# Optimization experiments

Hardware: AMD Instinct MI355X
Metric: run time of the kernel (lower is better)

Reference implementation:

```python
import jax, jax.numpy as jnp
import numpy as np

B, T, C, H = 2, 2048, 2048, 16
HD = C // H  # head dim = 128
ROPE_BASE = 10000.0


def apply_rope(x):
    # x: [B, T, H, HD]; interleaved-pair rotation as in torchtune RoPE
    t = x.shape[1]
    half = x.shape[-1] // 2
    theta = 1.0 / (ROPE_BASE ** (jnp.arange(0, HD, 2, dtype=jnp.float32) / HD))  # [HD/2]
    ang = jnp.arange(t, dtype=jnp.float32)[:, None] * theta[None, :]  # [T, HD/2]
    cos = jnp.cos(ang)[None, :, None, :]  # [1, T, 1, HD/2]
    sin = jnp.sin(ang)[None, :, None, :]
    xs = x.reshape(*x.shape[:-1], half, 2)  # [B,T,H,HD/2,2]
    x0, x1 = xs[..., 0], xs[..., 1]
    out = jnp.stack([x0 * cos - x1 * sin, x1 * cos + x0 * sin], axis=-1)
    return out.reshape(x.shape)


def setup_inputs() -> dict:
    key = jax.random.key(0)
    k1, k2, k3 = jax.random.split(key, 3)
    x = jax.random.normal(k1, (B, T, C), dtype=jnp.float32)
    attn_mask = jnp.tril(jnp.ones((T, T), dtype=bool))[None, None]  # causal [1,1,T,T]
    W_attn = jax.random.normal(k2, (3 * C, C), dtype=jnp.float32) * (C ** -0.5)
    W_proj = jax.random.normal(k3, (C, C), dtype=jnp.float32) * (C ** -0.5)
    return {"x": x, "attn_mask": attn_mask, "W_attn": W_attn, "W_proj": W_proj}


def reference(x, attn_mask, W_attn, W_proj):
    b, t, c = x.shape
    qkv = x @ W_attn.T  # [B,T,3C]
    q, k, v = jnp.split(qkv, 3, axis=-1)
    q = apply_rope(q.reshape(b, t, H, HD)).transpose(0, 2, 1, 3)  # [B,H,T,HD]
    k = apply_rope(k.reshape(b, t, H, HD)).transpose(0, 2, 1, 3)
    v = v.reshape(b, t, H, HD).transpose(0, 2, 1, 3)
    scale = 1.0 / jnp.sqrt(jnp.float32(HD))
    scores = jnp.einsum("bhqd,bhkd->bhqk", q, k) * scale
    scores = jnp.where(attn_mask, scores, jnp.finfo(scores.dtype).min)
    probs = jax.nn.softmax(scores, axis=-1)
    y = jnp.einsum("bhqk,bhkd->bhqd", probs, v)  # [B,H,T,HD]
    y = y.transpose(0, 2, 1, 3).reshape(b, t, c)
    return y @ W_proj.T
```

## Files before the change

kernel.cpp:

```cpp
#include <hip/hip_runtime.h>
#include <hip/hip_bf16.h>
#include <math.h>

typedef unsigned short u16;
typedef unsigned int   u32;
typedef __attribute__((ext_vector_type(8)))  short bf16x8;
typedef __attribute__((ext_vector_type(4)))  float f32x4;
typedef __attribute__((ext_vector_type(16))) float f32x16;

#define B_  2
#define T_  2048
#define C_  2048
#define H_  16
#define HD_ 128
#define M_  4096
#define N3C 6144

__device__ __forceinline__ float bf2f_lo(u32 u) { return __uint_as_float(u << 16); }
__device__ __forceinline__ float bf2f_hi(u32 u) { return __uint_as_float(u & 0xffff0000u); }

__device__ __forceinline__ u16 f2bf(float f) {
    u32 u = __float_as_uint(f);
    return (u16)((u + 0x7fffu + ((u >> 16) & 1u)) >> 16);
}
__device__ __forceinline__ u32 pack2(float a, float b) {
    return (u32)f2bf(a) | ((u32)f2bf(b) << 16);
}
__device__ __forceinline__ void store1(float* p, float v) { *p = v; }
__device__ __forceinline__ void store1(__hip_bfloat16* p, float v) { *(u16*)p = f2bf(v); }

__device__ __forceinline__ void gload16(const void* g, void* l) {
    __builtin_amdgcn_global_load_lds((__attribute__((address_space(1))) void*)g,
                                     (__attribute__((address_space(3))) void*)l, 16, 0, 0);
}

__global__ __launch_bounds__(256) void cvt_bf16(const float* __restrict__ in,
                                                u16* __restrict__ out, int n8) {
    const int i = blockIdx.x * 256 + threadIdx.x;
    if (i < n8) {
        const float4 a = ((const float4*)in)[2 * i];
        const float4 b = ((const float4*)in)[2 * i + 1];
        ((uint4*)out)[i] = make_uint4(pack2(a.x, a.y), pack2(a.z, a.w),
                                      pack2(b.x, b.y), pack2(b.z, b.w));
    }
}

template <typename TO>
__global__ __launch_bounds__(256, 3) void gemm_pipe(const __hip_bfloat16* __restrict__ A,
                                                    const __hip_bfloat16* __restrict__ W,
                                                    TO* __restrict__ Cout,
                                                    int N, int K, int gx) {
    __shared__ u16 As[3][128 * 32];
    __shared__ u16 Bs[3][128 * 32];
    const int nwg = gridDim.x * gridDim.y;
    const int id  = blockIdx.y * gx + blockIdx.x;
    const int swz = (id & 7) * (nwg >> 3) + (id >> 3);
    const int bm  = (swz / gx) * 128;
    const int bn  = (swz % gx) * 128;

    const int tid  = threadIdx.x;
    const int w    = tid >> 6;
    const int lane = tid & 63;
    const int g    = lane >> 4;
    const int c    = lane & 15;
    const int wr   = (w >> 1) * 64;
    const int wc   = (w & 1) * 64;

    const int srow = lane >> 2;
    const int scol = (lane & 3) * 8;
    const __hip_bfloat16* ga0 = A + (size_t)(bm + w * 32 + srow) * K + scol;
    const __hip_bfloat16* ga1 = ga0 + (size_t)16 * K;
    const __hip_bfloat16* gb0 = W + (size_t)(bn + w * 32 + srow) * K + scol;
    const __hip_bfloat16* gb1 = gb0 + (size_t)16 * K;

#define STAGE_(bi, kk) do {                                   \
        gload16(ga0 + (kk), &As[bi][w * 1024]);               \
        gload16(ga1 + (kk), &As[bi][w * 1024 + 512]);         \
        gload16(gb0 + (kk), &Bs[bi][w * 1024]);               \
        gload16(gb1 + (kk), &Bs[bi][w * 1024 + 512]);         \
    } while (0)

    f32x4 acc[4][4];
#pragma unroll
    for (int mi = 0; mi < 4; ++mi)
#pragma unroll
        for (int ni = 0; ni < 4; ++ni)
            acc[mi][ni] = (f32x4){0.f, 0.f, 0.f, 0.f};

    const int NT = K / 32;
    STAGE_(0, 0);
    STAGE_(1, 32);

    int cur = 0;
    for (int t = 0; t < NT; ++t) {
        if (t + 1 < NT) { asm volatile("s_waitcnt vmcnt(4)" ::: "memory"); }
        else            { asm volatile("s_waitcnt vmcnt(0)" ::: "memory"); }
        __builtin_amdgcn_sched_barrier(0);
        __builtin_amdgcn_s_barrier();
        __builtin_amdgcn_sched_barrier(0);

        if (t + 2 < NT) {
            const int nb = (cur + 2 >= 3) ? cur - 1 : cur + 2;
            STAGE_(nb, (t + 2) * 32);
        }

        bf16x8 af[4], bfr[4];
#pragma unroll
        for (int mi = 0; mi < 4; ++mi)
            af[mi] = *(const bf16x8*)&As[cur][(wr + mi * 16 + c) * 32 + g * 8];
#pragma unroll
        for (int ni = 0; ni < 4; ++ni)
            bfr[ni] = *(const bf16x8*)&Bs[cur][(wc + ni * 16 + c) * 32 + g * 8];

        __builtin_amdgcn_s_setprio(1);
#pragma unroll
        for (int mi = 0; mi < 4; ++mi)
#pragma unroll
            for (int ni = 0; ni < 4; ++ni)
                acc[mi][ni] = __builtin_amdgcn_mfma_f32_16x16x32_bf16(
                    af[mi], bfr[ni], acc[mi][ni], 0, 0, 0);
        __builtin_amdgcn_s_setprio(0);

        cur = (cur + 1 == 3) ? 0 : cur + 1;
    }
#undef STAGE_

#pragma unroll
    for (int mi = 0; mi < 4; ++mi)
#pragma unroll
        for (int ni = 0; ni < 4; ++ni)
#pragma unroll
            for (int i = 0; i < 4; ++i) {
                const int row = bm + wr + mi * 16 + 4 * g + i;
                const int col = bn + wc + ni * 16 + c;
                store1(Cout + (size_t)row * N + col, acc[mi][ni][i]);
            }
}

__device__ __forceinline__ void stage_tile(u16* dst, const float* src, int ldk, int tid) {
    const int r0  = tid >> 3;
    const int off = (tid & 7) * 4;
#pragma unroll
    for (int it = 0; it < 4; ++it) {
        const int row = r0 + it * 32;
        const float4 v = *(const float4*)(src + (size_t)row * ldk + off);
        *(uint2*)&dst[row * 40 + off] = make_uint2(pack2(v.x, v.y), pack2(v.z, v.w));
    }
}
__device__ __forceinline__ void stage_tile(u16* dst, const __hip_bfloat16* src, int ldk, int tid) {
    const int r0  = tid >> 2;
    const int off = (tid & 3) * 8;
#pragma unroll
    for (int it = 0; it < 2; ++it) {
        const int row = r0 + it * 64;
        *(uint4*)&dst[row * 40 + off] = *(const uint4*)(src + (size_t)row * ldk + off);
    }
}

template <typename TA, typename TW, typename TO>
__global__ __launch_bounds__(256) void gemm_mfma(const TA* __restrict__ A,
                                                 const TW* __restrict__ W,
                                                 TO* __restrict__ Cout,
                                                 int N, int K, int gx) {
    __shared__ u16 As[128 * 40];
    __shared__ u16 Bs[128 * 40];
    const int nwg = gridDim.x * gridDim.y;
    const int id  = blockIdx.y * gx + blockIdx.x;
    const int swz = (id & 7) * (nwg >> 3) + (id >> 3);
    const int bm  = (swz / gx) * 128;
    const int bn  = (swz % gx) * 128;

    const int tid  = threadIdx.x;
    const int w    = tid >> 6;
    const int lane = tid & 63;
    const int g    = lane >> 4;
    const int c    = lane & 15;
    const int wr   = (w >> 1) * 64;
    const int wc   = (w & 1) * 64;

    f32x4 acc[4][4];
#pragma unroll
    for (int mi = 0; mi < 4; ++mi)
#pragma unroll
        for (int ni = 0; ni < 4; ++ni)
            acc[mi][ni] = (f32x4){0.f, 0.f, 0.f, 0.f};

    const TA* Ab = A + (size_t)bm * K;
    const TW* Wb = W + (size_t)bn * K;

    for (int k0 = 0; k0 < K; k0 += 32) {
        __syncthreads();
        stage_tile(As, Ab + k0, K, tid);
        stage_tile(Bs, Wb + k0, K, tid);
        __syncthreads();

        bf16x8 af[4], bfr[4];
#pragma unroll
        for (int mi = 0; mi < 4; ++mi)
            af[mi] = *(const bf16x8*)&As[(wr + mi * 16 + c) * 40 + g * 8];
#pragma unroll
        for (int ni = 0; ni < 4; ++ni)
            bfr[ni] = *(const bf16x8*)&Bs[(wc + ni * 16 + c) * 40 + g * 8];
#pragma unroll
        for (int mi = 0; mi < 4; ++mi)
#pragma unroll
            for (int ni = 0; ni < 4; ++ni)
                acc[mi][ni] = __builtin_amdgcn_mfma_f32_16x16x32_bf16(
                    af[mi], bfr[ni], acc[mi][ni], 0, 0, 0);
    }

#pragma unroll
    for (int mi = 0; mi < 4; ++mi)
#pragma unroll
        for (int ni = 0; ni < 4; ++ni)
#pragma unroll
            for (int i = 0; i < 4; ++i) {
                const int row = bm + wr + mi * 16 + 4 * g + i;
                const int col = bn + wc + ni * 16 + c;
                store1(Cout + (size_t)row * N + col, acc[mi][ni][i]);
            }
}

__global__ __launch_bounds__(256) void rope_kernel(__hip_bfloat16* __restrict__ qkv) {
    const int id  = blockIdx.x * 256 + threadIdx.x;
    const int i   = id & 63;
    const int h   = (id >> 6) & (H_ - 1);
    const int qk  = (id >> 10) & 1;
    const int row = id >> 11;
    const int t   = row & (T_ - 1);
    const size_t base = (size_t)row * N3C + (size_t)qk * C_ + h * HD_ + 2 * i;
    u32* p = (u32*)((u16*)qkv + base);
    const u32 v = *p;
    const float x0 = bf2f_lo(v), x1 = bf2f_hi(v);
    const float l2th = 0.20762050593046f;
    const float theta = exp2f(-(float)i * l2th);
    const float ang = (float)t * theta;
    float s, cc;
    sincosf(ang, &s, &cc);
    *p = pack2(x0 * cc - x1 * s, x1 * cc + x0 * s);
}

__device__ __forceinline__ int PI_(int s) {
    return (s & 51) | ((s & 4) << 1) | ((s & 8) >> 1);
}

__global__ __launch_bounds__(256, 2) void attn_mfma2(const __hip_bfloat16* __restrict__ qkv,
                                                     __hip_bfloat16* __restrict__ y) {
    __shared__ u16 Ks[64 * 136];
    __shared__ u16 Vt[128 * 72];
    __shared__ float Red[128];

    const int tid  = threadIdx.x;
    const int w    = tid >> 6;
    const int lane = tid & 63;
    const int c31  = lane & 31;
    const int hi   = lane >> 5;
    const int bid  = blockIdx.x;
    const int bh   = bid & 31;
    const int qb   = 15 - (bid >> 5);
    const int b    = bh >> 4, h = bh & 15;
    const int q0   = qb * 128;

    const size_t base = (size_t)b * T_ * N3C + (size_t)h * HD_;
    const __hip_bfloat16* Qp = qkv + base;
    const __hip_bfloat16* Kp = qkv + base + C_;
    const __hip_bfloat16* Vp = qkv + base + 2 * C_;

    bf16x8 qf[8];
    {
        const size_t qoff = (size_t)(q0 + w * 32 + c31) * N3C + hi * 8;
#pragma unroll
        for (int kc = 0; kc < 8; ++kc)
            qf[kc] = *(const bf16x8*)(Qp + qoff + kc * 16);
    }

    f32x16 o[4];
#pragma unroll
    for (int db = 0; db < 4; ++db)
#pragma unroll
        for (int r = 0; r < 16; ++r) o[db][r] = 0.f;

    float m_ = -1e30f, l_ = 0.f;
    const int   myq   = q0 + w * 32 + c31;
    const float SCALE = 0.08838834764831845f;

    const int s_   = tid >> 2;
    const int dsub = tid & 3;
    const int vcol = PI_(s_) ^ (dsub << 4);

    uint4 kreg[4], vreg[4];
#pragma unroll
    for (int it = 0; it < 4; ++it) {
        const int col = dsub * 32 + it * 8;
        const size_t goff = (size_t)s_ * N3C + col;
        kreg[it] = *(const uint4*)(Kp + goff);
        vreg[it] = *(const uint4*)(Vp + goff);
    }

    const int nkt = 2 * qb + 2;
    for (int kt = 0; kt < nkt; ++kt) {
        __syncthreads();
#pragma unroll
        for (int it = 0; it < 4; ++it) {
            const int col = dsub * 32 + it * 8;
            *(uint4*)&Ks[s_ * 136 + col] = kreg[it];
            const u32 vw[4] = {vreg[it].x, vreg[it].y, vreg[it].z, vreg[it].w};
#pragma unroll
            for (int j = 0; j < 8; ++j)
                Vt[(col + j) * 72 + vcol] = (u16)(vw[j >> 1] >> ((j & 1) * 16));
        }
        if (kt + 1 < nkt) {
#pragma unroll
            for (int it = 0; it < 4; ++it) {
                const int col = dsub * 32 + it * 8;
                const size_t goff = (size_t)((kt + 1) * 64 + s_) * N3C + col;
                kreg[it] = *(const uint4*)(Kp + goff);
                vreg[it] = *(const uint4*)(Vp + goff);
            }
        }
        __syncthreads();

        const int k0 = kt * 64;
        f32x16 sA, sB;
#pragma unroll
        for (int r = 0; r < 16; ++r) { sA[r] = 0.f; sB[r] = 0.f; }
        __builtin_amdgcn_s_setprio(1);
#pragma unroll
        for (int kc = 0; kc < 8; ++kc) {
            const bf16x8 ka = *(const bf16x8*)&Ks[c31 * 136 + kc * 16 + hi * 8];
            sA = __builtin_amdgcn_mfma_f32_32x32x16_bf16(ka, qf[kc], sA, 0, 0, 0);
            const bf16x8 kb_ = *(const bf16x8*)&Ks[(32 + c31) * 136 + kc * 16 + hi * 8];
            sB = __builtin_amdgcn_mfma_f32_32x32x16_bf16(kb_, qf[kc], sB, 0, 0, 0);
        }
        __builtin_amdgcn_s_setprio(0);

        float pmax = -1e30f;
#pragma unroll
        for (int r = 0; r < 16; ++r) {
            const int cr = (r & 3) + 8 * (r >> 2) + 4 * hi;
            sA[r] = (k0 + cr      <= myq) ? sA[r] * SCALE : -1e30f;
            sB[r] = (k0 + 32 + cr <= myq) ? sB[r] * SCALE : -1e30f;
            pmax = fmaxf(pmax, fmaxf(sA[r], sB[r]));
        }
        pmax = fmaxf(pmax, __shfl_xor(pmax, 32));

        if (__any(pmax > m_ + 8.f)) {
            const float mn   = fmaxf(m_, pmax);
            const float corr = __expf(m_ - mn);
            Red[w * 32 + c31] = corr;
            float cf[16];
#pragma unroll
            for (int r = 0; r < 16; ++r)
                cf[r] = Red[w * 32 + ((r & 3) + 8 * (r >> 2) + 4 * hi)];
#pragma unroll
            for (int db = 0; db < 4; ++db)
#pragma unroll
                for (int r = 0; r < 16; ++r) o[db][r] *= cf[r];
            l_ *= corr;
            m_ = mn;
        }

        float psum = 0.f;
#pragma unroll
        for (int r = 0; r < 16; ++r) {
            sA[r] = __expf(sA[r] - m_); psum += sA[r];
            sB[r] = __expf(sB[r] - m_); psum += sB[r];
        }
        psum += __shfl_xor(psum, 32);
        l_ += psum;

        __builtin_amdgcn_s_setprio(1);
#pragma unroll
        for (int kb2 = 0; kb2 < 2; ++kb2) {
#pragma unroll
            for (int c2 = 0; c2 < 2; ++c2) {
                union { u32 u[4]; bf16x8 v; } pk;
#pragma unroll
                for (int q2 = 0; q2 < 4; ++q2) {
                    const int r = 8 * c2 + 2 * q2;
                    const float e0 = kb2 ? sB[r]     : sA[r];
                    const float e1 = kb2 ? sB[r + 1] : sA[r + 1];
                    pk.u[q2] = pack2(e0, e1);
                }
#pragma unroll
                for (int db = 0; db < 4; ++db) {
                    const int colb = (kb2 * 32 + c2 * 16 + hi * 8) ^ (db << 4);
                    const bf16x8 vb = *(const bf16x8*)&Vt[(db * 32 + c31) * 72 + colb];
                    o[db] = __builtin_amdgcn_mfma_f32_32x32x16_bf16(pk.v, vb, o[db], 0, 0, 0);
                }
            }
        }
        __builtin_amdgcn_s_setprio(0);
    }

    Red[w * 32 + c31] = l_;
    float lv[16];
#pragma unroll
    for (int r = 0; r < 16; ++r)
        lv[r] = 1.f / Red[w * 32 + ((r & 3) + 8 * (r >> 2) + 4 * hi)];
#pragma unroll
    for (int db = 0; db < 4; ++db)
#pragma unroll
        for (int r = 0; r < 16; ++r) {
            const int q = q0 + w * 32 + (r & 3) + 8 * (r >> 2) + 4 * hi;
            store1(y + (size_t)(b * T_ + q) * C_ + h * HD_ + db * 32 + c31,
                   o[db][r] * lv[r]);
        }
}

extern "C" void kernel_launch(void* const* d_in, const int* in_sizes, int n_in,
                              void* d_out, int out_size, void* d_ws, size_t ws_size,
                              hipStream_t stream) {
    const float* x  = (const float*)d_in[0];
    const float* Wa = (const float*)d_in[2];
    const float* Wp = (const float*)d_in[3];
    float* out = (float*)d_out;

    u16* ws = (u16*)d_ws;
    __hip_bfloat16* qkv = (__hip_bfloat16*)ws;
    __hip_bfloat16* y   = (__hip_bfloat16*)(ws + (size_t)M_ * N3C);

    const size_t NEED = ((size_t)M_ * N3C + (size_t)M_ * C_ +
                         (size_t)M_ * C_ +
                         (size_t)N3C * C_ + (size_t)C_ * C_) * 2;

    if (ws_size >= NEED) {
        u16* xb  = ws + (size_t)M_ * N3C + (size_t)M_ * C_;
        u16* Wab = xb + (size_t)M_ * C_;
        u16* Wpb = Wab + (size_t)N3C * C_;

        cvt_bf16<<<(M_ * C_ / 8 + 255) / 256, 256, 0, stream>>>(x, xb, M_ * C_ / 8);
        cvt_bf16<<<(N3C * C_ / 8 + 255) / 256, 256, 0, stream>>>(Wa, Wab, N3C * C_ / 8);
        cvt_bf16<<<(C_ * C_ / 8 + 255) / 256, 256, 0, stream>>>(Wp, Wpb, C_ * C_ / 8);

        gemm_pipe<__hip_bfloat16>
            <<<dim3(N3C / 128, M_ / 128), 256, 0, stream>>>(
                (const __hip_bfloat16*)xb, (const __hip_bfloat16*)Wab, qkv, N3C, C_, N3C / 128);
        rope_kernel<<<(M_ * C_) / 256, 256, 0, stream>>>(qkv);
        attn_mfma2<<<512, 256, 0, stream>>>(qkv, y);
        gemm_pipe<float>
            <<<dim3(C_ / 128, M_ / 128), 256, 0, stream>>>(
                y, (const __hip_bfloat16*)Wpb, out, C_, C_, C_ / 128);
    } else {
        gemm_mfma<float, float, __hip_bfloat16>
            <<<dim3(N3C / 128, M_ / 128), 256, 0, stream>>>(x, Wa, qkv, N3C, C_, N3C / 128);
        rope_kernel<<<(M_ * C_) / 256, 256, 0, stream>>>(qkv);
        attn_mfma2<<<512, 256, 0, stream>>>(qkv, y);
        gemm_mfma<__hip_bfloat16, float, float>
            <<<dim3(C_ / 128, M_ / 128), 256, 0, stream>>>(y, Wp, out, C_, C_, C_ / 128);
    }
}
```

Measured before the change: 307.3 us.

## Use 256x256-tile 512-thread GEMM for QKV projection and reorder attention blocks

Adds a new bf16 GEMM kernel with 256x256 output tiles and 8 waves per block, each wave owning a 128x64 sub-tile, with a three-stage LDS pipeline. It replaces the 128x128 kernel for the QKV projection. The goal is more data reuse per LDS load and less global traffic. The cost is 96KB of LDS per block, which likely limits a CU to one block. The 128-register accumulator may also cause register pressure, and 384 blocks give an uneven tail across CUs. Separately, the attention grid now runs the second half of its query blocks in ascending order to change the causal load-balance schedule.

```diff
diff --git a/kernel.cpp b/kernel.cpp
--- a/kernel.cpp
+++ b/kernel.cpp
@@ -43,6 +43,98 @@
         ((uint4*)out)[i] = make_uint4(pack2(a.x, a.y), pack2(a.z, a.w),
                                       pack2(b.x, b.y), pack2(b.z, b.w));
     }
+}
+
+template <typename TO>
+__global__ __launch_bounds__(512, 2) void gemm_pipe256(const __hip_bfloat16* __restrict__ A,
+                                                       const __hip_bfloat16* __restrict__ W,
+                                                       TO* __restrict__ Cout,
+                                                       int N, int K, int gx) {
+    __shared__ u16 As[3][256 * 32];
+    __shared__ u16 Bs[3][256 * 32];
+    const int nwg = gridDim.x * gridDim.y;
+    const int id  = blockIdx.y * gx + blockIdx.x;
+    const int swz = (id & 7) * (nwg >> 3) + (id >> 3);
+    const int bm  = (swz / gx) * 256;
+    const int bn  = (swz % gx) * 256;
+
+    const int tid  = threadIdx.x;
+    const int w    = tid >> 6;
+    const int lane = tid & 63;
+    const int g    = lane >> 4;
+    const int c    = lane & 15;
+    const int wr   = (w >> 2) * 128;
+    const int wc   = (w & 3) * 64;
+
+    const int srow = lane >> 2;
+    const int scol = (lane & 3) * 8;
+    const __hip_bfloat16* ga0 = A + (size_t)(bm + w * 32 + srow) * K + scol;
+    const __hip_bfloat16* ga1 = ga0 + (size_t)16 * K;
+    const __hip_bfloat16* gb0 = W + (size_t)(bn + w * 32 + srow) * K + scol;
+    const __hip_bfloat16* gb1 = gb0 + (size_t)16 * K;
+
+#define STAGE_(bi, kk) do {                                   \
+        gload16(ga0 + (kk), &As[bi][w * 1024]);               \
+        gload16(ga1 + (kk), &As[bi][w * 1024 + 512]);         \
+        gload16(gb0 + (kk), &Bs[bi][w * 1024]);               \
+        gload16(gb1 + (kk), &Bs[bi][w * 1024 + 512]);         \
+    } while (0)
+
+    f32x4 acc[8][4];
+#pragma unroll
+    for (int mi = 0; mi < 8; ++mi)
+#pragma unroll
+        for (int ni = 0; ni < 4; ++ni)
+            acc[mi][ni] = (f32x4){0.f, 0.f, 0.f, 0.f};
+
+    const int NT = K / 32;
+    STAGE_(0, 0);
+    STAGE_(1, 32);
+
+    int cur = 0;
+    for (int t = 0; t < NT; ++t) {
+        if (t + 1 < NT) { asm volatile("s_waitcnt vmcnt(4)" ::: "memory"); }
+        else            { asm volatile("s_waitcnt vmcnt(0)" ::: "memory"); }
+        __builtin_amdgcn_sched_barrier(0);
+        __builtin_amdgcn_s_barrier();
+        __builtin_amdgcn_sched_barrier(0);
+
+        if (t + 2 < NT) {
+            const int nb = (cur + 2 >= 3) ? cur - 1 : cur + 2;
+            STAGE_(nb, (t + 2) * 32);
+        }
+
+        bf16x8 af[8], bfr[4];
+#pragma unroll
+        for (int mi = 0; mi < 8; ++mi)
+            af[mi] = *(const bf16x8*)&As[cur][(wr + mi * 16 + c) * 32 + g * 8];
+#pragma unroll
+        for (int ni = 0; ni < 4; ++ni)
+            bfr[ni] = *(const bf16x8*)&Bs[cur][(wc + ni * 16 + c) * 32 + g * 8];
+
+        __builtin_amdgcn_s_setprio(1);
+#pragma unroll
+        for (int mi = 0; mi < 8; ++mi)
+#pragma unroll
+            for (int ni = 0; ni < 4; ++ni)
+                acc[mi][ni] = __builtin_amdgcn_mfma_f32_16x16x32_bf16(
+                    af[mi], bfr[ni], acc[mi][ni], 0, 0, 0);
+        __builtin_amdgcn_s_setprio(0);
+
+        cur = (cur + 1 == 3) ? 0 : cur + 1;
+    }
+#undef STAGE_
+
+#pragma unroll
+    for (int mi = 0; mi < 8; ++mi)
+#pragma unroll
+        for (int ni = 0; ni < 4; ++ni)
+#pragma unroll
+            for (int i = 0; i < 4; ++i) {
+                const int row = bm + wr + mi * 16 + 4 * g + i;
+                const int col = bn + wc + ni * 16 + c;
+                store1(Cout + (size_t)row * N + col, acc[mi][ni][i]);
+            }
 }
 
 template <typename TO>
@@ -257,7 +349,7 @@
     const int hi   = lane >> 5;
     const int bid  = blockIdx.x;
     const int bh   = bid & 31;
-    const int qb   = 15 - (bid >> 5);
+    const int qb   = (bid < 256) ? 15 - (bid >> 5) : (bid >> 5) - 8;
     const int b    = bh >> 4, h = bh & 15;
     const int q0   = qb * 128;
 
@@ -433,9 +525,9 @@
         cvt_bf16<<<(N3C * C_ / 8 + 255) / 256, 256, 0, stream>>>(Wa, Wab, N3C * C_ / 8);
         cvt_bf16<<<(C_ * C_ / 8 + 255) / 256, 256, 0, stream>>>(Wp, Wpb, C_ * C_ / 8);
 
-        gemm_pipe<__hip_bfloat16>
-            <<<dim3(N3C / 128, M_ / 128), 256, 0, stream>>>(
-                (const __hip_bfloat16*)xb, (const __hip_bfloat16*)Wab, qkv, N3C, C_, N3C / 128);
+        gemm_pipe256<__hip_bfloat16>
+            <<<dim3(N3C / 256, M_ / 256), 512, 0, stream>>>(
+                (const __hip_bfloat16*)xb, (const __hip_bfloat16*)Wab, qkv, N3C, C_, N3C / 256);
         rope_kernel<<<(M_ * C_) / 256, 256, 0, stream>>>(qkv);
         attn_mfma2<<<512, 256, 0, stream>>>(qkv, y);
         gemm_pipe<float>
```

Result: slower. 351.8 us (+14.5%).
